# Optimization experiments

Measured on AMD Instinct MI355X. Metric: run time of the kernel, lower is better.

The kernel has to match this reference:

```python
import jax, jax.numpy as jnp
from jax import lax
import numpy as np

D_IN = 12      # latent_dim / flow input_dim
HALF = 6       # coupling split
HID = 192      # flow_hidden_dim
LAYERS = 24    # flow_layers
N_BASES = 66
SYM = 12       # symmetry_dim
OUT_DIM = 6    # rows of tangent frame J_p
B = 16384
EPS_P = 1e-3
CLAMP = 2.0    # soft clamp for 'exp_clamp' scale map: s = CLAMP*tanh(raw/CLAMP)


def _mlp(z1, p):
    W1, b1, W2, b2, W3, b3 = p
    h = jax.nn.relu(z1 @ W1.T + b1)
    h = jax.nn.relu(h @ W2.T + b2)
    return h @ W3.T + b3


def _coupling_fwd(z, p):
    # AffineCouplingBlock (split->affine->merge) followed by Permute(swap)
    z1, z2 = z[..., :HALF], z[..., HALF:]
    prm = _mlp(z1, p)
    shift, sraw = prm[..., 0::2], prm[..., 1::2]
    s = CLAMP * jnp.tanh(sraw / CLAMP)
    z2 = z2 * jnp.exp(s) + shift
    # merge [z1, z2'] then swap halves -> [z2', z1]
    return jnp.concatenate([z2, z1], axis=-1), jnp.sum(s, axis=-1)


def _coupling_inv(z, p):
    # inverse of Permute(swap) is swap again
    z = jnp.concatenate([z[..., HALF:], z[..., :HALF]], axis=-1)
    z1, z2 = z[..., :HALF], z[..., HALF:]
    prm = _mlp(z1, p)
    shift, sraw = prm[..., 0::2], prm[..., 1::2]
    s = CLAMP * jnp.tanh(sraw / CLAMP)
    z2 = (z2 - shift) * jnp.exp(-s)
    return jnp.concatenate([z1, z2], axis=-1), -jnp.sum(s, axis=-1)


def flow_forward(z, params):
    def step(c, p):
        z, ld = c
        z, d = _coupling_fwd(z, p)
        return (z, ld + d), None
    (z, ld), _ = lax.scan(step, (z, jnp.zeros(z.shape[:-1], z.dtype)), params)
    return z, ld


def flow_inverse(y, params):
    def step(c, p):
        z, ld = c
        z, d = _coupling_inv(z, p)
        return (z, ld + d), None
    (z, ld), _ = lax.scan(step, (y, jnp.zeros(y.shape[:-1], y.dtype)), params, reverse=True)
    return z, ld


def pullback_tangent(z, v, params):
    # J[b] = v[b] @ d(flow_forward)/dz at z[b], via per-sample vjp
    def one(zb, vb):
        _, vjp_fn = jax.vjp(lambda zz: flow_forward(zz, params)[0], zb)
        return jax.vmap(lambda r: vjp_fn(r)[0])(vb)
    return jax.vmap(one)(z, v)


def kl_divergence(J_p, J_q, log_var_diag):
    b, out_dim, in_dim = J_p.shape
    J_p = J_p / jnp.sqrt(jnp.sum(J_p * J_p))  # global normalization
    S_p = jnp.einsum('bni,bmi->bnm', J_p, J_p)
    S_q = jnp.einsum('bin,bim->bnm', J_q, J_q)
    S_pq = jnp.einsum('bni,bmi->bnm', J_p[:, :, :SYM], J_q)
    D = jnp.exp(-log_var_diag)  # (in_dim,)
    I_p = jnp.eye(out_dim, dtype=J_p.dtype)
    I_q = jnp.eye(SYM, dtype=J_q.dtype)
    M = S_p + EPS_P * I_p
    H = S_q + D[:SYM] * I_q
    norm_M = jnp.maximum(jnp.mean(jnp.diagonal(M, axis1=-2, axis2=-1), -1), 1e-6)
    norm_H = jnp.maximum(jnp.mean(jnp.diagonal(H, axis1=-2, axis2=-1), -1), 1e-6)
    M = M + 1e-3 * norm_M[:, None, None] * I_p
    H = H + 1e-3 * norm_H[:, None, None] * I_q
    Db = D + 1e-3 * norm_H[:, None]  # (b, in_dim)
    trace_p = jnp.einsum('bij,bij,bj->b', J_p, J_p, Db)
    trace_q = jnp.einsum('bij,bij->b', J_q, J_q)
    trace_pq = jnp.einsum('bij,bij->b', S_pq, S_pq)
    trace = (EPS_P + 1e-3 * norm_M) * (jnp.sum(Db, -1) + trace_q) + trace_p + trace_pq
    L_M = jnp.linalg.cholesky(M)
    L_H = jnp.linalg.cholesky(H)
    logdet_M = 2.0 * jnp.sum(jnp.log(jnp.diagonal(L_M, axis1=-2, axis2=-1)), -1)
    logdet_H = 2.0 * jnp.sum(jnp.log(jnp.diagonal(L_H, axis1=-2, axis2=-1)), -1)
    logdet_p = logdet_M + (in_dim - out_dim) * np.float32(np.log(EPS_P))
    logdet_q = logdet_H + jnp.sum(jnp.log(Db[:, SYM:]), -1)
    logdet = -(logdet_p + logdet_q)
    return 0.5 * (trace + logdet - in_dim)


def setup_inputs() -> dict:
    key = jax.random.key(0)
    ks = jax.random.split(key, 10)
    y = jax.random.normal(ks[0], (B, D_IN), jnp.float32)
    J_p = jax.random.normal(ks[1], (B, OUT_DIM, D_IN), jnp.float32)
    sc = 0.05
    W1 = sc * jax.random.normal(ks[2], (LAYERS, HID, HALF), jnp.float32)
    b1 = sc * jax.random.normal(ks[3], (LAYERS, HID), jnp.float32)
    W2 = sc * jax.random.normal(ks[4], (LAYERS, HID, HID), jnp.float32)
    b2 = sc * jax.random.normal(ks[5], (LAYERS, HID), jnp.float32)
    W3 = sc * jax.random.normal(ks[6], (LAYERS, D_IN, HID), jnp.float32)
    b3 = sc * jax.random.normal(ks[7], (LAYERS, D_IN), jnp.float32)
    Wsym = (1.0 / np.sqrt(SYM)) * jax.random.normal(ks[8], (N_BASES, SYM, SYM), jnp.float32)
    log_var_diag = jnp.zeros((D_IN,), jnp.float32)
    return {"y": y, "J_p": J_p, "W1": W1, "b1": b1, "W2": W2, "b2": b2,
            "W3": W3, "b3": b3, "Wsym": Wsym, "log_var_diag": log_var_diag}


def reference(y, J_p, W1, b1, W2, b2, W3, b3, Wsym, log_var_diag):
    params = (W1, b1, W2, b2, W3, b3)
    z, ld = flow_inverse(y, params)
    # DiagGaussian(trainable=False) base log prob = standard normal
    log_prob = ld - 0.5 * D_IN * np.float32(np.log(2.0 * np.pi)) - 0.5 * jnp.sum(z * z, -1)
    Jp = pullback_tangent(z, J_p, params)
    A = Wsym - jnp.swapaxes(Wsym, -1, -2)
    J_q = jnp.einsum('bi,mji->bmj', z[:, :SYM], A)
    kl = kl_divergence(Jp, J_q, log_var_diag)
    return (log_prob, kl)
```

## Files before the change

kernel.cpp:

```cpp
#include <hip/hip_runtime.h>
#include <hip/hip_bf16.h>
#include <math.h>

#define BTOT   16384
#define NLAYER 24
#define HID    192
#define NDIN   12
#define NBASE  66
#define EPSP   1e-3f
#define EPB    32

#define EST 200
#define W3ST 17
#define OB_H1  0
#define OB_G   12800
#define OB_R   89600
#define OB_W1  98816
#define OB_W3F 101888
#define OB_PRM 114944
#define OB_GZ  118016
#define OB_Z1  122624
#define OB_LD  123392
#define OB_ZQ  123520
#define OB_RED 123648
#define SMEM_BYTES 123680

typedef __attribute__((ext_vector_type(8))) short s8v;
typedef __attribute__((ext_vector_type(4))) float f4v;
#define MFMA16(a,b,c) __builtin_amdgcn_mfma_f32_16x16x32_bf16(a,b,c,0,0,0)

__device__ __forceinline__ unsigned short f2bf(float f) {
  unsigned u = __builtin_bit_cast(unsigned, f);
  u += 0x7fffu + ((u >> 16) & 1u);
  return (unsigned short)(u >> 16);
}
__device__ __forceinline__ float bf2f(unsigned short h) {
  unsigned u = ((unsigned)h) << 16;
  return __builtin_bit_cast(float, u);
}
__device__ __forceinline__ unsigned pk2(float a, float b) {
  return (unsigned)f2bf(a) | ((unsigned)f2bf(b) << 16);
}
__device__ __forceinline__ float blo(unsigned u) { return bf2f((unsigned short)(u & 0xffff)); }
__device__ __forceinline__ float bhi(unsigned u) { return bf2f((unsigned short)(u >> 16)); }

__global__ void prep_kernel(const float* __restrict__ W2,
                            unsigned short* __restrict__ w2b,
                            unsigned short* __restrict__ w2t) {
  int idx = blockIdx.x * 256 + threadIdx.x;
  int l   = idx / (HID * HID);
  int rem = idx - l * HID * HID;
  int k   = rem / HID;
  int j   = rem - k * HID;
  w2b[idx] = f2bf(W2[idx]);
  w2t[idx] = f2bf(W2[l * HID * HID + j * HID + k]);
}

__global__ __launch_bounds__(768) void flow_kernel(
    float* __restrict__ yz, float* __restrict__ jp,
    const float* __restrict__ W1, const float* __restrict__ b1,
    const float* __restrict__ b2,
    const float* __restrict__ W3, const float* __restrict__ b3,
    const unsigned short* __restrict__ w2b,
    const unsigned short* __restrict__ w2t,
    float* __restrict__ ws_sum, float* __restrict__ out_lp) {
  extern __shared__ char smraw[];
  unsigned short* sH1b = (unsigned short*)(smraw + OB_H1);
  unsigned short* sGb  = (unsigned short*)(smraw + OB_G);
  float* sW3f = (float*)(smraw + OB_W3F);
  float* sR   = (float*)(smraw + OB_R);
  float* sPRM = (float*)(smraw + OB_PRM);
  float* sGZ  = (float*)(smraw + OB_GZ);
  float* sZ1  = (float*)(smraw + OB_Z1);
  float* sLD  = (float*)(smraw + OB_LD);
  float* sZQ  = (float*)(smraw + OB_ZQ);
  float* sRed = (float*)(smraw + OB_RED);

  const int tid  = threadIdx.x;
  const int lane = tid & 63;
  const int w    = __builtin_amdgcn_readfirstlane(tid >> 6);
  const int e    = tid & 31;
  const int grp  = tid >> 5;
  const int lm   = lane & 15, lq = lane >> 4;
  const int blk  = blockIdx.x;

  float z_a = 0.f, z_b = 0.f;
  if (tid < 192) {
    int i = grp;
    z_a = yz[(blk * EPB + e) * 12 + i];
    z_b = yz[(blk * EPB + e) * 12 + 6 + i];
    sZ1[i * EPB + e] = z_b;
  }
  if (tid < 32) { sLD[tid] = 0.f; sZQ[tid] = 0.f; }
  if (tid == 0) sRed[0] = 0.f;
  for (int idx = tid; idx < 1152; idx += 768) sGZ[idx] = 0.f;
  if (tid < 768) sPRM[tid] = 0.f;
  for (int idx = tid; idx < 72 * EPB; idx += 768) {
    int rt = idx >> 5, ee = idx & 31;
    sR[idx] = jp[(blk * EPB + ee) * 72 + rt];
  }
  __syncthreads();

  for (int l = NLAYER - 1; l >= 0; --l) {
    const float* W1l = W1 + l * HID * 6;
    const float* b1l = b1 + l * HID;
    const float* b2l = b2 + l * HID;
    const float* W3l = W3 + l * NDIN * HID;
    const float* b3l = b3 + l * NDIN;
    const unsigned short* w2bl = w2b + l * HID * HID;
    const unsigned short* w2tl = w2t + l * HID * HID;
    float* cur = sPRM + (l & 1) * 384;
    float* prv = sPRM + ((l + 1) & 1) * 384;

    if (tid < 192) {
      const float* wr = W1l + tid * 6;
      uint4 pk;
      pk.x = pk2(wr[0], wr[1]); pk.y = pk2(wr[2], wr[3]);
      pk.z = pk2(wr[4], wr[5]); pk.w = 0;
      *(uint4*)(smraw + OB_W1 + tid * 16) = pk;
    }
    for (int idx = tid; idx < 2304; idx += 768) {
      int t = idx / 192, j = idx - t * 192;
      sW3f[j * W3ST + t] = W3l[idx];
    }
    if (tid < 384) cur[tid] = 0.f;
    if (l != NLAYER - 1) {
      for (int idx = tid; idx < 1152; idx += 768) {
        int i = idx / 192, rem = idx - i * 192;
        int r = rem >> 5, e5 = rem & 31;
        float r1  = sR[(r * 12 + i) * EPB + e5];
        float r2o = sR[(r * 12 + 6 + i) * EPB + e5];
        float es  = prv[(2 * i + 1) * EPB + e5];
        sR[(r * 12 + i) * EPB + e5]     = r2o + sGZ[i * 192 + rem];
        sR[(r * 12 + 6 + i) * EPB + e5] = r1 * es;
        sGZ[i * 192 + rem] = 0.f;
      }
    }
    {
      float z1v[6];
      #pragma unroll
      for (int i = 0; i < 6; ++i) z1v[i] = sZ1[i * EPB + e];
      int jb8 = grp * 8;
      #pragma unroll
      for (int jj = 0; jj < 8; ++jj) {
        int j = jb8 + jj;
        float acc = b1l[j];
        #pragma unroll
        for (int i = 0; i < 6; ++i) acc = fmaf(W1l[j * 6 + i], z1v[i], acc);
        sH1b[e * EST + j] = f2bf(fmaxf(acc, 0.f));
      }
    }
    __syncthreads();

    {
      f4v acc2[2] = {{0,0,0,0},{0,0,0,0}};
      #pragma unroll 2
      for (int kk = 0; kk < 6; ++kk) {
        int jo = kk * 32 + lq * 8;
        s8v A  = *(const s8v*)(w2bl + (w * 16 + lm) * HID + jo);
        s8v B0 = *(const s8v*)&sH1b[lm * EST + jo];
        s8v B1 = *(const s8v*)&sH1b[(16 + lm) * EST + jo];
        acc2[0] = MFMA16(A, B0, acc2[0]);
        acc2[1] = MFMA16(A, B1, acc2[1]);
      }
      int jb2 = w * 16 + lq * 4;
      float pp[2][12];
      #pragma unroll
      for (int nt = 0; nt < 2; ++nt)
        #pragma unroll
        for (int t = 0; t < 12; ++t) pp[nt][t] = 0.f;
      #pragma unroll
      for (int nt = 0; nt < 2; ++nt) {
        int e2 = nt * 16 + lm;
        float hv[4];
        #pragma unroll
        for (int rg = 0; rg < 4; ++rg)
          hv[rg] = fmaxf(acc2[nt][rg] + b2l[jb2 + rg], 0.f);
        unsigned* dst = (unsigned*)sGb + ((e2 * EST + jb2) >> 1);
        dst[0] = pk2(hv[0], hv[1]);
        dst[1] = pk2(hv[2], hv[3]);
        #pragma unroll
        for (int rg = 0; rg < 4; ++rg) {
          const float* w3r = sW3f + (jb2 + rg) * W3ST;
          float v = hv[rg];
          #pragma unroll
          for (int t = 0; t < 12; ++t) pp[nt][t] = fmaf(w3r[t], v, pp[nt][t]);
        }
      }
      #pragma unroll
      for (int nt = 0; nt < 2; ++nt)
        #pragma unroll
        for (int t = 0; t < 12; ++t) {
          float v = pp[nt][t];
          v += __shfl_xor(v, 16);
          v += __shfl_xor(v, 32);
          if (lane < 16) atomicAdd(&cur[t * EPB + nt * 16 + lane], v);
        }
    }
    __syncthreads();

    if (tid < 192) {
      int i = grp;
      float sh = b3l[2 * i]     + cur[(2 * i) * EPB + e];
      float sr = b3l[2 * i + 1] + cur[(2 * i + 1) * EPB + e];
      float s  = 2.f * tanhf(0.5f * sr);
      float es = expf(s), en = expf(-s);
      float tv = z_a - sh;
      z_a = z_b;
      z_b = tv * en;
      sZ1[i * EPB + e] = z_b;
      cur[(2 * i) * EPB + e]     = tv * (1.f - 0.25f * s * s);
      cur[(2 * i + 1) * EPB + e] = es;
      atomicAdd(&sLD[e], -s);
    }
    __syncthreads();

    {
      float tf[6];
      #pragma unroll
      for (int i = 0; i < 6; ++i) tf[i] = cur[(2 * i) * EPB + e];
      int slab = grp * 8;
      const unsigned* hp = (const unsigned*)&sGb[e * EST + slab];
      unsigned h2d[4];
      #pragma unroll
      for (int c = 0; c < 4; ++c) h2d[c] = hp[c];
      float weff[8][6];
      #pragma unroll
      for (int jj = 0; jj < 8; ++jj) {
        const float* wrow = sW3f + (slab + jj) * W3ST;
        #pragma unroll
        for (int c = 0; c < 6; ++c)
          weff[jj][c] = fmaf(tf[c], wrow[2 * c + 1], wrow[2 * c]);
      }
      #pragma unroll
      for (int r = 0; r < 6; ++r) {
        float g[8];
        #pragma unroll
        for (int jj = 0; jj < 8; ++jj) g[jj] = 0.f;
        #pragma unroll
        for (int c = 0; c < 6; ++c) {
          float r1 = sR[(r * 12 + c) * EPB + e];
          #pragma unroll
          for (int jj = 0; jj < 8; ++jj)
            g[jj] = fmaf(weff[jj][c], r1, g[jj]);
        }
        unsigned* dst = (unsigned*)sGb + (((r * EPB + e) * EST + slab) >> 1);
        #pragma unroll
        for (int pr = 0; pr < 4; ++pr) {
          float v0 = (h2d[pr] & 0xffffu) ? g[2 * pr] : 0.f;
          float v1 = (h2d[pr] >> 16)     ? g[2 * pr + 1] : 0.f;
          dst[pr] = pk2(v0, v1);
        }
      }
    }
    __syncthreads();

    {
      const int mtg3 = (w & 3) * 3;
      const int ntg4 = (w >> 2) * 4;
      f4v acc[3][4] = {{{0,0,0,0},{0,0,0,0},{0,0,0,0},{0,0,0,0}},
                       {{0,0,0,0},{0,0,0,0},{0,0,0,0},{0,0,0,0}},
                       {{0,0,0,0},{0,0,0,0},{0,0,0,0},{0,0,0,0}}};
      #pragma unroll 2
      for (int kk = 0; kk < 6; ++kk) {
        int jo = kk * 32 + lq * 8;
        s8v A[3], B[4];
        #pragma unroll
        for (int p = 0; p < 3; ++p)
          A[p] = *(const s8v*)(w2tl + ((mtg3 + p) * 16 + lm) * HID + jo);
        #pragma unroll
        for (int q = 0; q < 4; ++q)
          B[q] = *(const s8v*)&sGb[((ntg4 + q) * 16 + lm) * EST + jo];
        #pragma unroll
        for (int p = 0; p < 3; ++p)
          #pragma unroll
          for (int q = 0; q < 4; ++q)
            acc[p][q] = MFMA16(A[p], B[q], acc[p][q]);
      }
      float pz[4][6];
      #pragma unroll
      for (int q = 0; q < 4; ++q)
        #pragma unroll
        for (int i = 0; i < 6; ++i) pz[q][i] = 0.f;
      #pragma unroll
      for (int p = 0; p < 3; ++p) {
        int kb = (mtg3 + p) * 16 + lq * 4;
        float w1v[4][6];
        #pragma unroll
        for (int rg = 0; rg < 4; ++rg) {
          uint4 wr = *(const uint4*)(smraw + OB_W1 + (kb + rg) * 16);
          w1v[rg][0] = blo(wr.x); w1v[rg][1] = bhi(wr.x);
          w1v[rg][2] = blo(wr.y); w1v[rg][3] = bhi(wr.y);
          w1v[rg][4] = blo(wr.z); w1v[rg][5] = bhi(wr.z);
        }
        #pragma unroll
        for (int q = 0; q < 4; ++q) {
          int e31 = (((ntg4 + q) & 1) << 4) + lm;
          const unsigned* mp = (const unsigned*)&sH1b[e31 * EST + kb];
          unsigned mm0 = mp[0], mm1 = mp[1];
          unsigned short hb[4] = {
            (unsigned short)(mm0 & 0xffff), (unsigned short)(mm0 >> 16),
            (unsigned short)(mm1 & 0xffff), (unsigned short)(mm1 >> 16)};
          #pragma unroll
          for (int rg = 0; rg < 4; ++rg) {
            float val = hb[rg] ? acc[p][q][rg] : 0.f;
            #pragma unroll
            for (int i = 0; i < 6; ++i)
              pz[q][i] = fmaf(w1v[rg][i], val, pz[q][i]);
          }
        }
      }
      #pragma unroll
      for (int q = 0; q < 4; ++q)
        #pragma unroll
        for (int i = 0; i < 6; ++i) {
          float v = pz[q][i];
          v += __shfl_xor(v, 16);
          v += __shfl_xor(v, 32);
          if (lane < 16) atomicAdd(&sGZ[i * 192 + (ntg4 + q) * 16 + lane], v);
        }
    }
    __syncthreads();
  }

  {
    float* prv0 = sPRM;
    for (int idx = tid; idx < 1152; idx += 768) {
      int i = idx / 192, rem = idx - i * 192;
      int r = rem >> 5, e5 = rem & 31;
      float r1  = sR[(r * 12 + i) * EPB + e5];
      float r2o = sR[(r * 12 + 6 + i) * EPB + e5];
      float es  = prv0[(2 * i + 1) * EPB + e5];
      sR[(r * 12 + i) * EPB + e5]     = r2o + sGZ[i * 192 + rem];
      sR[(r * 12 + 6 + i) * EPB + e5] = r1 * es;
    }
  }
  if (tid < 192) {
    int i = grp;
    yz[(blk * EPB + e) * 12 + i]     = z_a;
    yz[(blk * EPB + e) * 12 + 6 + i] = z_b;
    atomicAdd(&sZQ[e], fmaf(z_a, z_a, z_b * z_b));
  }
  __syncthreads();
  if (tid < 32)
    out_lp[blk * EPB + tid] = sLD[tid] - 11.027262398456072f - 0.5f * sZQ[tid];

  float part = 0.f;
  for (int idx = tid; idx < 72 * EPB; idx += 768) {
    int rt = idx >> 5, ee = idx & 31;
    float v = sR[idx];
    jp[(blk * EPB + ee) * 72 + rt] = v;
    part = fmaf(v, v, part);
  }
  #pragma unroll
  for (int off = 32; off > 0; off >>= 1) part += __shfl_down(part, off, 64);
  if ((tid & 63) == 0) atomicAdd(&sRed[0], part);
  __syncthreads();
  if (tid == 0) atomicAdd(ws_sum, sRed[0]);
}

__global__ __launch_bounds__(256) void kl_kernel(
    const float* __restrict__ zin, const float* __restrict__ jpin,
    const float* __restrict__ Wsym, const float* __restrict__ lvd,
    const float* __restrict__ ws_sum, float* __restrict__ out_kl) {
  int elem = blockIdx.x * 256 + threadIdx.x;
  float z[12];
  #pragma unroll
  for (int i = 0; i < 12; ++i) z[i] = zin[elem * 12 + i];
  float scale = 1.0f / sqrtf(ws_sum[0]);
  float Jp[6][12];
  #pragma unroll
  for (int n = 0; n < 6; ++n)
    #pragma unroll
    for (int j = 0; j < 12; ++j)
      Jp[n][j] = jpin[elem * 72 + n * 12 + j] * scale;

  float Sq[78];
  #pragma unroll
  for (int i = 0; i < 78; ++i) Sq[i] = 0.f;
  float tq = 0.f, tpq = 0.f;

  for (int m = 0; m < NBASE; ++m) {
    const float* Wm = Wsym + m * 144;
    float jq[12];
    #pragma unroll
    for (int j = 0; j < 12; ++j) {
      float acc = 0.f;
      #pragma unroll
      for (int i = 0; i < 12; ++i)
        acc = fmaf(Wm[j * 12 + i] - Wm[i * 12 + j], z[i], acc);
      jq[j] = acc;
    }
    #pragma unroll
    for (int i = 0; i < 12; ++i) {
      tq = fmaf(jq[i], jq[i], tq);
      #pragma unroll
      for (int j = 0; j <= i; ++j)
        Sq[i * (i + 1) / 2 + j] = fmaf(jq[i], jq[j], Sq[i * (i + 1) / 2 + j]);
    }
    #pragma unroll
    for (int n = 0; n < 6; ++n) {
      float d = 0.f;
      #pragma unroll
      for (int j = 0; j < 12; ++j) d = fmaf(Jp[n][j], jq[j], d);
      tpq = fmaf(d, d, tpq);
    }
  }

  float Dv[12], Db[12];
  #pragma unroll
  for (int j = 0; j < 12; ++j) Dv[j] = expf(-lvd[j]);

  float mh = 0.f;
  #pragma unroll
  for (int i = 0; i < 12; ++i) mh += Sq[i * (i + 1) / 2 + i] + Dv[i];
  float norm_H = fmaxf(mh * (1.f / 12.f), 1e-6f);
  #pragma unroll
  for (int i = 0; i < 12; ++i) Sq[i * (i + 1) / 2 + i] += Dv[i] + 1e-3f * norm_H;
  float sumDb = 0.f;
  #pragma unroll
  for (int j = 0; j < 12; ++j) { Db[j] = Dv[j] + 1e-3f * norm_H; sumDb += Db[j]; }

  float M[21];
  #pragma unroll
  for (int n = 0; n < 6; ++n)
    #pragma unroll
    for (int mm = 0; mm <= n; ++mm) {
      float acc = 0.f;
      #pragma unroll
      for (int j = 0; j < 12; ++j) acc = fmaf(Jp[n][j], Jp[mm][j], acc);
      M[n * (n + 1) / 2 + mm] = acc;
    }
  float md = 0.f;
  #pragma unroll
  for (int i = 0; i < 6; ++i) md += M[i * (i + 1) / 2 + i];
  float norm_M = fmaxf(md * (1.f / 6.f) + EPSP, 1e-6f);
  #pragma unroll
  for (int i = 0; i < 6; ++i) M[i * (i + 1) / 2 + i] += EPSP + 1e-3f * norm_M;

  float trace_p = 0.f;
  #pragma unroll
  for (int n = 0; n < 6; ++n)
    #pragma unroll
    for (int j = 0; j < 12; ++j)
      trace_p = fmaf(Jp[n][j] * Jp[n][j], Db[j], trace_p);

  float trace = (EPSP + 1e-3f * norm_M) * (sumDb + tq) + trace_p + tpq;

  float ldM = 0.f;
  #pragma unroll
  for (int jc = 0; jc < 6; ++jc) {
    float d = M[jc * (jc + 1) / 2 + jc];
    #pragma unroll
    for (int k = 0; k < jc; ++k) d -= M[jc * (jc + 1) / 2 + k] * M[jc * (jc + 1) / 2 + k];
    d = sqrtf(d);
    ldM += logf(d);
    float di = 1.f / d;
    M[jc * (jc + 1) / 2 + jc] = d;
    #pragma unroll
    for (int i2 = jc + 1; i2 < 6; ++i2) {
      float v = M[i2 * (i2 + 1) / 2 + jc];
      #pragma unroll
      for (int k = 0; k < jc; ++k) v -= M[i2 * (i2 + 1) / 2 + k] * M[jc * (jc + 1) / 2 + k];
      M[i2 * (i2 + 1) / 2 + jc] = v * di;
    }
  }

  float ldH = 0.f;
  #pragma unroll
  for (int jc = 0; jc < 12; ++jc) {
    float d = Sq[jc * (jc + 1) / 2 + jc];
    #pragma unroll
    for (int k = 0; k < jc; ++k) d -= Sq[jc * (jc + 1) / 2 + k] * Sq[jc * (jc + 1) / 2 + k];
    d = sqrtf(d);
    ldH += logf(d);
    float di = 1.f / d;
    Sq[jc * (jc + 1) / 2 + jc] = d;
    #pragma unroll
    for (int i2 = jc + 1; i2 < 12; ++i2) {
      float v = Sq[i2 * (i2 + 1) / 2 + jc];
      #pragma unroll
      for (int k = 0; k < jc; ++k) v -= Sq[i2 * (i2 + 1) / 2 + k] * Sq[jc * (jc + 1) / 2 + k];
      Sq[i2 * (i2 + 1) / 2 + jc] = v * di;
    }
  }

  float logdet_p = 2.f * ldM + 6.f * logf(EPSP);
  float logdet_q = 2.f * ldH;
  out_kl[elem] = 0.5f * (trace - (logdet_p + logdet_q) - 12.f);
}

extern "C" void kernel_launch(void* const* d_in, const int* in_sizes, int n_in,
                              void* d_out, int out_size, void* d_ws, size_t ws_size,
                              hipStream_t stream) {
  (void)in_sizes; (void)n_in; (void)out_size; (void)ws_size;
  float* y    = (float*)d_in[0];
  float* Jp   = (float*)d_in[1];
  const float* W1   = (const float*)d_in[2];
  const float* b1   = (const float*)d_in[3];
  const float* W2   = (const float*)d_in[4];
  const float* b2   = (const float*)d_in[5];
  const float* W3   = (const float*)d_in[6];
  const float* b3   = (const float*)d_in[7];
  const float* Wsym = (const float*)d_in[8];
  const float* lvd  = (const float*)d_in[9];
  float* out = (float*)d_out;

  float* ws_sum = (float*)d_ws;
  unsigned short* w2b = (unsigned short*)((char*)d_ws + 256);
  unsigned short* w2t = (unsigned short*)((char*)d_ws + 256 +
                                          NLAYER * HID * HID * 2);
  hipMemsetAsync(d_ws, 0, 4, stream);

  hipFuncSetAttribute((const void*)flow_kernel,
                      hipFuncAttributeMaxDynamicSharedMemorySize, SMEM_BYTES);

  prep_kernel<<<3456, 256, 0, stream>>>(W2, w2b, w2t);
  flow_kernel<<<BTOT / EPB, 768, SMEM_BYTES, stream>>>(
      y, Jp, W1, b1, b2, W3, b3, w2b, w2t, ws_sum, out);
  kl_kernel<<<64, 256, 0, stream>>>(y, Jp, Wsym, lvd, ws_sum, out + BTOT);
}
```

Baseline: 1.837 ms.

## Process 64 elements per block, with bitmask ReLU and two-half backward pass

Doubles the elements per block from 32 to 64, so each loaded layer's W2/W3/W1 weights are reused across twice as many samples in the forward MFMA, and the grid halves. The layer-2 ReLU activity is kept as a packed bitmask in shared memory instead of being read back from the bf16 activations. The backward gradient staging and MFMA pass run in two halves of 32 elements to fit the existing sGb buffer. Shared memory rises to about 156KB and each layer gains an extra barrier pair, which may lower occupancy or add sync cost.

```diff
diff --git a/kernel.cpp b/kernel.cpp
--- a/kernel.cpp
+++ b/kernel.cpp
@@ -8,22 +8,23 @@
 #define NDIN   12
 #define NBASE  66
 #define EPSP   1e-3f
-#define EPB    32
+#define EPB    64
 
 #define EST 200
 #define W3ST 17
 #define OB_H1  0
-#define OB_G   12800
-#define OB_R   89600
-#define OB_W1  98816
-#define OB_W3F 101888
-#define OB_PRM 114944
-#define OB_GZ  118016
-#define OB_Z1  122624
-#define OB_LD  123392
-#define OB_ZQ  123520
-#define OB_RED 123648
-#define SMEM_BYTES 123680
+#define OB_G   25600
+#define OB_M2  102400
+#define OB_R   104448
+#define OB_W1  122880
+#define OB_W3F 125952
+#define OB_PRM 139008
+#define OB_GZ  145152
+#define OB_Z1  154368
+#define OB_LD  155904
+#define OB_ZQ  156160
+#define OB_RED 156416
+#define SMEM_BYTES 156448
 
 typedef __attribute__((ext_vector_type(8))) short s8v;
 typedef __attribute__((ext_vector_type(4))) float f4v;
@@ -67,6 +68,7 @@
   extern __shared__ char smraw[];
   unsigned short* sH1b = (unsigned short*)(smraw + OB_H1);
   unsigned short* sGb  = (unsigned short*)(smraw + OB_G);
+  unsigned* sM2 = (unsigned*)(smraw + OB_M2);
   float* sW3f = (float*)(smraw + OB_W3F);
   float* sR   = (float*)(smraw + OB_R);
   float* sPRM = (float*)(smraw + OB_PRM);
@@ -79,24 +81,22 @@
   const int tid  = threadIdx.x;
   const int lane = tid & 63;
   const int w    = __builtin_amdgcn_readfirstlane(tid >> 6);
-  const int e    = tid & 31;
-  const int grp  = tid >> 5;
   const int lm   = lane & 15, lq = lane >> 4;
   const int blk  = blockIdx.x;
 
   float z_a = 0.f, z_b = 0.f;
-  if (tid < 192) {
-    int i = grp;
+  if (tid < 384) {
+    int i = tid >> 6, e = tid & 63;
     z_a = yz[(blk * EPB + e) * 12 + i];
     z_b = yz[(blk * EPB + e) * 12 + 6 + i];
     sZ1[i * EPB + e] = z_b;
   }
-  if (tid < 32) { sLD[tid] = 0.f; sZQ[tid] = 0.f; }
+  if (tid < 64) { sLD[tid] = 0.f; sZQ[tid] = 0.f; }
   if (tid == 0) sRed[0] = 0.f;
-  for (int idx = tid; idx < 1152; idx += 768) sGZ[idx] = 0.f;
-  if (tid < 768) sPRM[tid] = 0.f;
+  for (int idx = tid; idx < 2304; idx += 768) sGZ[idx] = 0.f;
+  sPRM[tid] = 0.f; sPRM[768 + tid] = 0.f;
   for (int idx = tid; idx < 72 * EPB; idx += 768) {
-    int rt = idx >> 5, ee = idx & 31;
+    int rt = idx >> 6, ee = idx & 63;
     sR[idx] = jp[(blk * EPB + ee) * 72 + rt];
   }
   __syncthreads();
@@ -109,8 +109,8 @@
     const float* b3l = b3 + l * NDIN;
     const unsigned short* w2bl = w2b + l * HID * HID;
     const unsigned short* w2tl = w2t + l * HID * HID;
-    float* cur = sPRM + (l & 1) * 384;
-    float* prv = sPRM + ((l + 1) & 1) * 384;
+    float* cur = sPRM + (l & 1) * 768;
+    float* prv = sPRM + ((l + 1) & 1) * 768;
 
     if (tid < 192) {
       const float* wr = W1l + tid * 6;
@@ -123,27 +123,29 @@
       int t = idx / 192, j = idx - t * 192;
       sW3f[j * W3ST + t] = W3l[idx];
     }
-    if (tid < 384) cur[tid] = 0.f;
+    cur[tid] = 0.f;
+    if (tid < 512) sM2[tid] = 0u;
     if (l != NLAYER - 1) {
-      for (int idx = tid; idx < 1152; idx += 768) {
-        int i = idx / 192, rem = idx - i * 192;
-        int r = rem >> 5, e5 = rem & 31;
-        float r1  = sR[(r * 12 + i) * EPB + e5];
-        float r2o = sR[(r * 12 + 6 + i) * EPB + e5];
-        float es  = prv[(2 * i + 1) * EPB + e5];
-        sR[(r * 12 + i) * EPB + e5]     = r2o + sGZ[i * 192 + rem];
-        sR[(r * 12 + 6 + i) * EPB + e5] = r1 * es;
-        sGZ[i * 192 + rem] = 0.f;
+      for (int idx = tid; idx < 2304; idx += 768) {
+        int i = idx / 384, rem = idx - i * 384;
+        int r = rem >> 6, eg = rem & 63;
+        float r1  = sR[(r * 12 + i) * EPB + eg];
+        float r2o = sR[(r * 12 + 6 + i) * EPB + eg];
+        float es  = prv[(2 * i + 1) * EPB + eg];
+        sR[(r * 12 + i) * EPB + eg]     = r2o + sGZ[i * 384 + rem];
+        sR[(r * 12 + 6 + i) * EPB + eg] = r1 * es;
+        sGZ[i * 384 + rem] = 0.f;
       }
     }
     {
+      int e = tid & 63, g12 = tid >> 6;
       float z1v[6];
       #pragma unroll
       for (int i = 0; i < 6; ++i) z1v[i] = sZ1[i * EPB + e];
-      int jb8 = grp * 8;
-      #pragma unroll
-      for (int jj = 0; jj < 8; ++jj) {
-        int j = jb8 + jj;
+      int jb = g12 * 16;
+      #pragma unroll
+      for (int jj = 0; jj < 16; ++jj) {
+        int j = jb + jj;
         float acc = b1l[j];
         #pragma unroll
         for (int i = 0; i < 6; ++i) acc = fmaf(W1l[j * 6 + i], z1v[i], acc);
@@ -153,54 +155,55 @@
     __syncthreads();
 
     {
-      f4v acc2[2] = {{0,0,0,0},{0,0,0,0}};
+      f4v acc4[4] = {{0,0,0,0},{0,0,0,0},{0,0,0,0},{0,0,0,0}};
       #pragma unroll 2
       for (int kk = 0; kk < 6; ++kk) {
         int jo = kk * 32 + lq * 8;
-        s8v A  = *(const s8v*)(w2bl + (w * 16 + lm) * HID + jo);
-        s8v B0 = *(const s8v*)&sH1b[lm * EST + jo];
-        s8v B1 = *(const s8v*)&sH1b[(16 + lm) * EST + jo];
-        acc2[0] = MFMA16(A, B0, acc2[0]);
-        acc2[1] = MFMA16(A, B1, acc2[1]);
+        s8v A = *(const s8v*)(w2bl + (w * 16 + lm) * HID + jo);
+        #pragma unroll
+        for (int nt = 0; nt < 4; ++nt) {
+          s8v B = *(const s8v*)&sH1b[(nt * 16 + lm) * EST + jo];
+          acc4[nt] = MFMA16(A, B, acc4[nt]);
+        }
       }
       int jb2 = w * 16 + lq * 4;
-      float pp[2][12];
-      #pragma unroll
-      for (int nt = 0; nt < 2; ++nt)
-        #pragma unroll
-        for (int t = 0; t < 12; ++t) pp[nt][t] = 0.f;
-      #pragma unroll
-      for (int nt = 0; nt < 2; ++nt) {
+      float bb[4];
+      #pragma unroll
+      for (int rg = 0; rg < 4; ++rg) bb[rg] = b2l[jb2 + rg];
+      #pragma unroll
+      for (int nt = 0; nt < 4; ++nt) {
         int e2 = nt * 16 + lm;
         float hv[4];
-        #pragma unroll
-        for (int rg = 0; rg < 4; ++rg)
-          hv[rg] = fmaxf(acc2[nt][rg] + b2l[jb2 + rg], 0.f);
-        unsigned* dst = (unsigned*)sGb + ((e2 * EST + jb2) >> 1);
-        dst[0] = pk2(hv[0], hv[1]);
-        dst[1] = pk2(hv[2], hv[3]);
+        unsigned nib = 0;
+        #pragma unroll
+        for (int rg = 0; rg < 4; ++rg) {
+          hv[rg] = fmaxf(acc4[nt][rg] + bb[rg], 0.f);
+          nib |= (hv[rg] > 0.f ? 1u : 0u) << rg;
+        }
+        atomicOr(&sM2[e2 * 8 + (jb2 >> 5)], nib << (jb2 & 31));
+        float pp[12];
+        #pragma unroll
+        for (int t = 0; t < 12; ++t) pp[t] = 0.f;
         #pragma unroll
         for (int rg = 0; rg < 4; ++rg) {
           const float* w3r = sW3f + (jb2 + rg) * W3ST;
           float v = hv[rg];
           #pragma unroll
-          for (int t = 0; t < 12; ++t) pp[nt][t] = fmaf(w3r[t], v, pp[nt][t]);
-        }
-      }
-      #pragma unroll
-      for (int nt = 0; nt < 2; ++nt)
+          for (int t = 0; t < 12; ++t) pp[t] = fmaf(w3r[t], v, pp[t]);
+        }
         #pragma unroll
         for (int t = 0; t < 12; ++t) {
-          float v = pp[nt][t];
+          float v = pp[t];
           v += __shfl_xor(v, 16);
           v += __shfl_xor(v, 32);
           if (lane < 16) atomicAdd(&cur[t * EPB + nt * 16 + lane], v);
         }
+      }
     }
     __syncthreads();
 
-    if (tid < 192) {
-      int i = grp;
+    if (tid < 384) {
+      int i = tid >> 6, e = tid & 63;
       float sh = b3l[2 * i]     + cur[(2 * i) * EPB + e];
       float sr = b3l[2 * i + 1] + cur[(2 * i + 1) * EPB + e];
       float s  = 2.f * tanhf(0.5f * sr);
@@ -215,139 +218,144 @@
     }
     __syncthreads();
 
-    {
-      float tf[6];
-      #pragma unroll
-      for (int i = 0; i < 6; ++i) tf[i] = cur[(2 * i) * EPB + e];
-      int slab = grp * 8;
-      const unsigned* hp = (const unsigned*)&sGb[e * EST + slab];
-      unsigned h2d[4];
-      #pragma unroll
-      for (int c = 0; c < 4; ++c) h2d[c] = hp[c];
-      float weff[8][6];
-      #pragma unroll
-      for (int jj = 0; jj < 8; ++jj) {
-        const float* wrow = sW3f + (slab + jj) * W3ST;
-        #pragma unroll
-        for (int c = 0; c < 6; ++c)
-          weff[jj][c] = fmaf(tf[c], wrow[2 * c + 1], wrow[2 * c]);
+    #pragma unroll 1
+    for (int h = 0; h < 2; ++h) {
+      {
+        int e_l = tid & 31, sl8 = tid >> 5, slab = sl8 * 8;
+        int e_g = h * 32 + e_l;
+        float tf6[6];
+        #pragma unroll
+        for (int i = 0; i < 6; ++i) tf6[i] = cur[(2 * i) * EPB + e_g];
+        unsigned m8 = (sM2[e_g * 8 + (sl8 >> 2)] >> ((sl8 & 3) * 8)) & 0xffu;
+        float weff[8][6];
+        #pragma unroll
+        for (int jj = 0; jj < 8; ++jj) {
+          const float* wrow = sW3f + (slab + jj) * W3ST;
+          #pragma unroll
+          for (int c = 0; c < 6; ++c)
+            weff[jj][c] = fmaf(tf6[c], wrow[2 * c + 1], wrow[2 * c]);
+        }
+        #pragma unroll
+        for (int r = 0; r < 6; ++r) {
+          float g[8];
+          #pragma unroll
+          for (int jj = 0; jj < 8; ++jj) g[jj] = 0.f;
+          #pragma unroll
+          for (int c = 0; c < 6; ++c) {
+            float r1 = sR[(r * 12 + c) * EPB + e_g];
+            #pragma unroll
+            for (int jj = 0; jj < 8; ++jj)
+              g[jj] = fmaf(weff[jj][c], r1, g[jj]);
+          }
+          unsigned* dst = (unsigned*)sGb + (((r * 32 + e_l) * EST + slab) >> 1);
+          #pragma unroll
+          for (int pr = 0; pr < 4; ++pr) {
+            float v0 = ((m8 >> (2 * pr)) & 1u)     ? g[2 * pr] : 0.f;
+            float v1 = ((m8 >> (2 * pr + 1)) & 1u) ? g[2 * pr + 1] : 0.f;
+            dst[pr] = pk2(v0, v1);
+          }
+        }
       }
-      #pragma unroll
-      for (int r = 0; r < 6; ++r) {
-        float g[8];
-        #pragma unroll
-        for (int jj = 0; jj < 8; ++jj) g[jj] = 0.f;
-        #pragma unroll
-        for (int c = 0; c < 6; ++c) {
-          float r1 = sR[(r * 12 + c) * EPB + e];
-          #pragma unroll
-          for (int jj = 0; jj < 8; ++jj)
-            g[jj] = fmaf(weff[jj][c], r1, g[jj]);
-        }
-        unsigned* dst = (unsigned*)sGb + (((r * EPB + e) * EST + slab) >> 1);
-        #pragma unroll
-        for (int pr = 0; pr < 4; ++pr) {
-          float v0 = (h2d[pr] & 0xffffu) ? g[2 * pr] : 0.f;
-          float v1 = (h2d[pr] >> 16)     ? g[2 * pr + 1] : 0.f;
-          dst[pr] = pk2(v0, v1);
-        }
+      __syncthreads();
+
+      {
+        const int mtg3 = (w & 3) * 3;
+        const int ntg4 = (w >> 2) * 4;
+        f4v acc[3][4] = {{{0,0,0,0},{0,0,0,0},{0,0,0,0},{0,0,0,0}},
+                         {{0,0,0,0},{0,0,0,0},{0,0,0,0},{0,0,0,0}},
+                         {{0,0,0,0},{0,0,0,0},{0,0,0,0},{0,0,0,0}}};
+        #pragma unroll 2
+        for (int kk = 0; kk < 6; ++kk) {
+          int jo = kk * 32 + lq * 8;
+          s8v A[3], B[4];
+          #pragma unroll
+          for (int p = 0; p < 3; ++p)
+            A[p] = *(const s8v*)(w2tl + ((mtg3 + p) * 16 + lm) * HID + jo);
+          #pragma unroll
+          for (int q = 0; q < 4; ++q)
+            B[q] = *(const s8v*)&sGb[((ntg4 + q) * 16 + lm) * EST + jo];
+          #pragma unroll
+          for (int p = 0; p < 3; ++p)
+            #pragma unroll
+            for (int q = 0; q < 4; ++q)
+              acc[p][q] = MFMA16(A[p], B[q], acc[p][q]);
+        }
+        float pz[4][6];
+        #pragma unroll
+        for (int q = 0; q < 4; ++q)
+          #pragma unroll
+          for (int i = 0; i < 6; ++i) pz[q][i] = 0.f;
+        #pragma unroll
+        for (int p = 0; p < 3; ++p) {
+          int kb = (mtg3 + p) * 16 + lq * 4;
+          float w1v[4][6];
+          #pragma unroll
+          for (int rg = 0; rg < 4; ++rg) {
+            uint4 wr = *(const uint4*)(smraw + OB_W1 + (kb + rg) * 16);
+            w1v[rg][0] = blo(wr.x); w1v[rg][1] = bhi(wr.x);
+            w1v[rg][2] = blo(wr.y); w1v[rg][3] = bhi(wr.y);
+            w1v[rg][4] = blo(wr.z); w1v[rg][5] = bhi(wr.z);
+          }
+          #pragma unroll
+          for (int q = 0; q < 4; ++q) {
+            int e_l = (((ntg4 + q) & 1) << 4) + lm;
+            const unsigned* mp =
+              (const unsigned*)&sH1b[(h * 32 + e_l) * EST + kb];
+            unsigned mm0 = mp[0], mm1 = mp[1];
+            unsigned short hb[4] = {
+              (unsigned short)(mm0 & 0xffff), (unsigned short)(mm0 >> 16),
+              (unsigned short)(mm1 & 0xffff), (unsigned short)(mm1 >> 16)};
+            #pragma unroll
+            for (int rg = 0; rg < 4; ++rg) {
+              float val = hb[rg] ? acc[p][q][rg] : 0.f;
+              #pragma unroll
+              for (int i = 0; i < 6; ++i)
+                pz[q][i] = fmaf(w1v[rg][i], val, pz[q][i]);
+            }
+          }
+        }
+        #pragma unroll
+        for (int q = 0; q < 4; ++q)
+          #pragma unroll
+          for (int i = 0; i < 6; ++i) {
+            float v = pz[q][i];
+            v += __shfl_xor(v, 16);
+            v += __shfl_xor(v, 32);
+            if (lane < 16) {
+              int col = (ntg4 + q) * 16 + lane;
+              atomicAdd(&sGZ[i * 384 + (col >> 5) * 64 + h * 32 + (col & 31)], v);
+            }
+          }
       }
-    }
-    __syncthreads();
-
-    {
-      const int mtg3 = (w & 3) * 3;
-      const int ntg4 = (w >> 2) * 4;
-      f4v acc[3][4] = {{{0,0,0,0},{0,0,0,0},{0,0,0,0},{0,0,0,0}},
-                       {{0,0,0,0},{0,0,0,0},{0,0,0,0},{0,0,0,0}},
-                       {{0,0,0,0},{0,0,0,0},{0,0,0,0},{0,0,0,0}}};
-      #pragma unroll 2
-      for (int kk = 0; kk < 6; ++kk) {
-        int jo = kk * 32 + lq * 8;
-        s8v A[3], B[4];
-        #pragma unroll
-        for (int p = 0; p < 3; ++p)
-          A[p] = *(const s8v*)(w2tl + ((mtg3 + p) * 16 + lm) * HID + jo);
-        #pragma unroll
-        for (int q = 0; q < 4; ++q)
-          B[q] = *(const s8v*)&sGb[((ntg4 + q) * 16 + lm) * EST + jo];
-        #pragma unroll
-        for (int p = 0; p < 3; ++p)
-          #pragma unroll
-          for (int q = 0; q < 4; ++q)
-            acc[p][q] = MFMA16(A[p], B[q], acc[p][q]);
-      }
-      float pz[4][6];
-      #pragma unroll
-      for (int q = 0; q < 4; ++q)
-        #pragma unroll
-        for (int i = 0; i < 6; ++i) pz[q][i] = 0.f;
-      #pragma unroll
-      for (int p = 0; p < 3; ++p) {
-        int kb = (mtg3 + p) * 16 + lq * 4;
-        float w1v[4][6];
-        #pragma unroll
-        for (int rg = 0; rg < 4; ++rg) {
-          uint4 wr = *(const uint4*)(smraw + OB_W1 + (kb + rg) * 16);
-          w1v[rg][0] = blo(wr.x); w1v[rg][1] = bhi(wr.x);
-          w1v[rg][2] = blo(wr.y); w1v[rg][3] = bhi(wr.y);
-          w1v[rg][4] = blo(wr.z); w1v[rg][5] = bhi(wr.z);
-        }
-        #pragma unroll
-        for (int q = 0; q < 4; ++q) {
-          int e31 = (((ntg4 + q) & 1) << 4) + lm;
-          const unsigned* mp = (const unsigned*)&sH1b[e31 * EST + kb];
-          unsigned mm0 = mp[0], mm1 = mp[1];
-          unsigned short hb[4] = {
-            (unsigned short)(mm0 & 0xffff), (unsigned short)(mm0 >> 16),
-            (unsigned short)(mm1 & 0xffff), (unsigned short)(mm1 >> 16)};
-          #pragma unroll
-          for (int rg = 0; rg < 4; ++rg) {
-            float val = hb[rg] ? acc[p][q][rg] : 0.f;
-            #pragma unroll
-            for (int i = 0; i < 6; ++i)
-              pz[q][i] = fmaf(w1v[rg][i], val, pz[q][i]);
-          }
-        }
-      }
-      #pragma unroll
-      for (int q = 0; q < 4; ++q)
-        #pragma unroll
-        for (int i = 0; i < 6; ++i) {
-          float v = pz[q][i];
-          v += __shfl_xor(v, 16);
-          v += __shfl_xor(v, 32);
-          if (lane < 16) atomicAdd(&sGZ[i * 192 + (ntg4 + q) * 16 + lane], v);
-        }
-    }
-    __syncthreads();
+      __syncthreads();
+    }
   }
 
   {
     float* prv0 = sPRM;
-    for (int idx = tid; idx < 1152; idx += 768) {
-      int i = idx / 192, rem = idx - i * 192;
-      int r = rem >> 5, e5 = rem & 31;
-      float r1  = sR[(r * 12 + i) * EPB + e5];
-      float r2o = sR[(r * 12 + 6 + i) * EPB + e5];
-      float es  = prv0[(2 * i + 1) * EPB + e5];
-      sR[(r * 12 + i) * EPB + e5]     = r2o + sGZ[i * 192 + rem];
-      sR[(r * 12 + 6 + i) * EPB + e5] = r1 * es;
-    }
-  }
-  if (tid < 192) {
-    int i = grp;
+    for (int idx = tid; idx < 2304; idx += 768) {
+      int i = idx / 384, rem = idx - i * 384;
+      int r = rem >> 6, eg = rem & 63;
+      float r1  = sR[(r * 12 + i) * EPB + eg];
+      float r2o = sR[(r * 12 + 6 + i) * EPB + eg];
+      float es  = prv0[(2 * i + 1) * EPB + eg];
+      sR[(r * 12 + i) * EPB + eg]     = r2o + sGZ[i * 384 + rem];
+      sR[(r * 12 + 6 + i) * EPB + eg] = r1 * es;
+    }
+  }
+  if (tid < 384) {
+    int i = tid >> 6, e = tid & 63;
     yz[(blk * EPB + e) * 12 + i]     = z_a;
     yz[(blk * EPB + e) * 12 + 6 + i] = z_b;
     atomicAdd(&sZQ[e], fmaf(z_a, z_a, z_b * z_b));
   }
   __syncthreads();
-  if (tid < 32)
+  if (tid < 64)
     out_lp[blk * EPB + tid] = sLD[tid] - 11.027262398456072f - 0.5f * sZQ[tid];
 
   float part = 0.f;
   for (int idx = tid; idx < 72 * EPB; idx += 768) {
-    int rt = idx >> 5, ee = idx & 31;
+    int rt = idx >> 6, ee = idx & 63;
     float v = sR[idx];
     jp[(blk * EPB + ee) * 72 + rt] = v;
     part = fmaf(v, v, part);
```

Result: no change. 1.867 ms (+1.6%).
